# Kernel optimization log

Hardware: AMD Instinct MI355X
Metric: run time of the kernel (lower is better)

The kernel has to match this reference:

```python
import jax, jax.numpy as jnp
import numpy as np

# Geometry of the single LocallyConnected2d layer being decomposed
FACTOR = 2      # number of sublayers the out_channels are split into
KH = KW = 3     # kernel size
DH = DW = 1     # stride
OH = OW = 32    # output spatial size
B, C_IN, C_OUT = 128, 32, 64
H = W = OH + KH - 1  # 34 (valid unfold with stride 1)


def setup_inputs() -> dict:
    key = jax.random.key(0)
    kx, kw_, kb = jax.random.split(key, 3)
    x = jax.random.normal(kx, (B, C_IN, H, W), dtype=jnp.float32)
    # per-location weights: (out_ch, in_ch, oh, ow, kh*kw) -- no weight sharing
    weight = jax.random.normal(kw_, (C_OUT, C_IN, OH, OW, KH * KW), dtype=jnp.float32) * 0.05
    bias = jax.random.normal(kb, (C_OUT, OH, OW), dtype=jnp.float32)
    return {"x": x, "weight": weight, "bias": bias}


def _unfold(x):
    # x: (B, C, H, W) -> patches: (B, C, OH, OW, KH*KW)
    # equivalent to torch x.unfold(2,kh,dh).unfold(3,kw,dw).reshape(..., kh*kw)
    cols = [x[:, :, i:i + DH * OH:DH, j:j + DW * OW:DW]
            for i in range(KH) for j in range(KW)]
    return jnp.stack(cols, axis=-1)


def reference(x, weight, bias):
    patches = _unfold(x)  # (B, C, OH, OW, K2)
    new_ch = weight.shape[0] // FACTOR
    outs = []
    for g in range(FACTOR):  # decomposed sublayers, concatenated on channel dim
        w_g = weight[g * new_ch:(g + 1) * new_ch]
        b_g = bias[g * new_ch:(g + 1) * new_ch]
        # out[b,o,i,j] = sum_{c,k} patches[b,c,i,j,k] * w[o,c,i,j,k] + b[o,i,j]
        o_g = jnp.einsum('bcijk,ocijk->boij', patches, w_g) + b_g[None]
        outs.append(o_g)
    return jnp.concatenate(outs, axis=1)  # (B, C_OUT, OH, OW)
```

## Files before the change

kernel.cpp:

```cpp
#include <hip/hip_runtime.h>
#include <cstdint>
#include <cstddef>

#define B_    128
#define C_    32
#define O_    64
#define H_    34
#define NPOS  1024
#define K9    9
#define BC    (B_ * C_)
#define BO    (B_ * O_)
#define NPK   (NPOS * K9)

typedef __bf16 v8bf __attribute__((ext_vector_type(8)));
typedef float  v4f  __attribute__((ext_vector_type(4)));
typedef float  f4a  __attribute__((ext_vector_type(4)));

__device__ __forceinline__ unsigned short f2bf(float f) {
    union { float f; unsigned int u; } v; v.f = f;
    unsigned int u = v.u;
    return (unsigned short)((u + 0x7FFFu + ((u >> 16) & 1u)) >> 16);
}

__global__ __launch_bounds__(256) void repack_x(const float* __restrict__ x,
                                                unsigned short* __restrict__ x2) {
    const int bq = blockIdx.x / 17;
    const int hp = blockIdx.x % 17;
    const int b0 = bq * 2;
    const int h0 = hp * 2;
    __shared__ unsigned short tile[2][H_][66];
    const int t = threadIdx.x;

    for (int e = t; e < 2176; e += 256) {
        const int bb  = e / 1088;
        const int rem = e % 1088;
        const int c   = rem / 34;
        const int wp  = rem % 34;
        const float2 v = *(const float2*)(x +
            ((size_t)((b0 + bb) * C_ + c) * H_ + h0) * H_ + wp * 2);
        const int hh = (wp >= 17) ? 1 : 0;
        const int w  = wp * 2 - hh * 34;
        const int idx = bb * 32 + c;
        tile[hh][w][idx]     = f2bf(v.x);
        tile[hh][w + 1][idx] = f2bf(v.y);
    }
    __syncthreads();

    for (int e = t; e < 2176; e += 256) {
        const int hh  = e / 1088;
        const int rem = e % 1088;
        const int w   = rem >> 5;
        const int i2  = rem & 31;
        ushort2 pk;
        pk.x = tile[hh][w][i2 * 2];
        pk.y = tile[hh][w][i2 * 2 + 1];
        *(ushort2*)(x2 + (size_t)((h0 + hh) * H_ + w) * BC + bq * 64 + i2 * 2) = pk;
    }
}

__global__ __launch_bounds__(256, 4) void lc_fused3(const unsigned short* __restrict__ x2,
                                                    const float* __restrict__ weight,
                                                    const float* __restrict__ bias,
                                                    float* __restrict__ out) {
    __shared__ __align__(16) unsigned short Wl[36 * 512];

    const int bid = blockIdx.x;
    const int lb  = (bid & 7) * 128 + (bid >> 3);
    const int i   = lb >> 5;
    const int jq  = (lb >> 3) & 3;
    const int oq  = (lb >> 1) & 3;
    const int bh  = lb & 1;
    const int j0  = jq * 8;
    const int o0  = oq * 16;
    const int posbase = i * 32 + j0;
    const int t = threadIdx.x;

    const int wv = t >> 6;
    const int l  = t & 63;
    const int lm = l & 15;
    const int q  = l >> 4;

    v4f acc[8];
#pragma unroll
    for (int a = 0; a < 8; ++a) acc[a] = (v4f){0.f, 0.f, 0.f, 0.f};

    const float* wbase = weight + ((size_t)(o0 * C_) * NPOS + posbase) * K9;

#pragma unroll
    for (int jjh = 0; jjh < 2; ++jjh) {
        const float* wb = wbase + jjh * 36;
#pragma unroll
        for (int g = 0; g < 2; ++g) {
            f4a v[9];
#pragma unroll
            for (int r = 0; r < 9; ++r) {
                const int idx = (g * 9 + r) * 256 + t;
                const int pl  = idx / 9;
                const int d4  = idx % 9;
                v[r] = *(const f4a*)(wb + (size_t)pl * NPK + d4 * 4);
            }
#pragma unroll
            for (int r = 0; r < 9; ++r) {
                const int idx = (g * 9 + r) * 256 + t;
                const int pl  = idx / 9;
                const int d4  = idx % 9;
                const int col = ((pl >> 3) ^ (d4 & 7)) * 8 + (pl & 7);
#pragma unroll
                for (int u = 0; u < 4; ++u)
                    Wl[(d4 * 4 + u) * 512 + col] = f2bf(v[r][u]);
            }
        }
        __syncthreads();

#pragma unroll
        for (int kh = 0; kh < 3; ++kh) {
            v8bf ax[6];
            const int rowbase = (i + kh) * H_ + j0 + jjh * 4;
#pragma unroll
            for (int w6 = 0; w6 < 6; ++w6) {
                const unsigned short* xrow = x2 + (size_t)(rowbase + w6) * BC;
                ax[w6] = *(const v8bf*)(xrow + (bh * 64 + wv * 16 + lm) * C_ + q * 8);
            }
#pragma unroll
            for (int kw = 0; kw < 3; ++kw) {
                const int tap = kh * 3 + kw;
#pragma unroll
                for (int jj = 0; jj < 4; ++jj) {
                    const int jk = jj * K9 + tap;
                    const int gc = ((lm * 4 + q) ^ ((jk >> 2) & 7)) * 8;
                    const v8bf bfr = *(const v8bf*)&Wl[jk * 512 + gc];
                    acc[jjh * 4 + jj] = __builtin_amdgcn_mfma_f32_16x16x32_bf16(
                        ax[kw + jj], bfr, acc[jjh * 4 + jj], 0, 0, 0);
                }
            }
        }
        if (jjh == 0) __syncthreads();
    }

    const float* bp = bias + (size_t)(o0 + lm) * NPOS + posbase;
    const f4a bv0 = *(const f4a*)bp;
    const f4a bv1 = *(const f4a*)(bp + 4);
#pragma unroll
    for (int r2 = 0; r2 < 4; ++r2) {
        const int b = bh * 64 + wv * 16 + q * 4 + r2;
        float* op = out + ((size_t)b * O_ + (o0 + lm)) * NPOS + posbase;
        f4a lo = {acc[0][r2] + bv0[0], acc[1][r2] + bv0[1],
                  acc[2][r2] + bv0[2], acc[3][r2] + bv0[3]};
        f4a hi = {acc[4][r2] + bv1[0], acc[5][r2] + bv1[1],
                  acc[6][r2] + bv1[2], acc[7][r2] + bv1[3]};
        *(f4a*)op       = lo;
        *(f4a*)(op + 4) = hi;
    }
}

__global__ __launch_bounds__(256) void lc_fallback(const float* __restrict__ x,
                                                   const float* __restrict__ weight,
                                                   const float* __restrict__ bias,
                                                   float* __restrict__ out) {
    const int pos = blockIdx.x;
    const int i = pos >> 5, j = pos & 31;
    const int t  = threadIdx.x;
    const int wv = t >> 6;
    const int l  = t & 63;
    const int lm = l & 15;
    const int q  = l >> 4;

    float bv[4];
#pragma unroll
    for (int nt = 0; nt < 4; ++nt)
        bv[nt] = bias[(size_t)(nt * 16 + lm) * NPOS + pos];

    v4f acc[2][4];
#pragma unroll
    for (int a = 0; a < 2; ++a)
#pragma unroll
        for (int n = 0; n < 4; ++n) acc[a][n] = (v4f){0.f, 0.f, 0.f, 0.f};

    for (int k = 0; k < K9; ++k) {
        const int kh = k / 3, kw = k % 3;
        v8bf af[2], bfr[4];
#pragma unroll
        for (int mt = 0; mt < 2; ++mt) {
            const int b = wv * 32 + mt * 16 + lm;
            union { v8bf v; unsigned short s[8]; } u;
#pragma unroll
            for (int cc = 0; cc < 8; ++cc)
                u.s[cc] = f2bf(x[(((size_t)b * C_ + q * 8 + cc) * H_ + (i + kh)) * H_ + (j + kw)]);
            af[mt] = u.v;
        }
#pragma unroll
        for (int nt = 0; nt < 4; ++nt) {
            union { v8bf v; unsigned short s[8]; } u;
#pragma unroll
            for (int cc = 0; cc < 8; ++cc) {
                const int p = (nt * 16 + lm) * C_ + q * 8 + cc;
                u.s[cc] = f2bf(weight[((size_t)p * NPOS + pos) * K9 + k]);
            }
            bfr[nt] = u.v;
        }
#pragma unroll
        for (int mt = 0; mt < 2; ++mt)
#pragma unroll
            for (int nt = 0; nt < 4; ++nt)
                acc[mt][nt] = __builtin_amdgcn_mfma_f32_16x16x32_bf16(
                    af[mt], bfr[nt], acc[mt][nt], 0, 0, 0);
    }
#pragma unroll
    for (int mt = 0; mt < 2; ++mt)
#pragma unroll
        for (int nt = 0; nt < 4; ++nt) {
            const int o = nt * 16 + lm;
#pragma unroll
            for (int r = 0; r < 4; ++r) {
                const int b = wv * 32 + mt * 16 + q * 4 + r;
                out[(size_t)(b * O_ + o) * NPOS + pos] = acc[mt][nt][r] + bv[nt];
            }
        }
}

extern "C" void kernel_launch(void* const* d_in, const int* in_sizes, int n_in,
                              void* d_out, int out_size, void* d_ws, size_t ws_size,
                              hipStream_t stream) {
    const float* x      = (const float*)d_in[0];
    const float* weight = (const float*)d_in[1];
    const float* bias   = (const float*)d_in[2];
    float* out          = (float*)d_out;

    const size_t X2B = (size_t)H_ * H_ * BC * sizeof(unsigned short);

    if (ws_size >= X2B) {
        unsigned short* x2 = (unsigned short*)d_ws;
        repack_x<<<64 * 17, 256, 0, stream>>>(x, x2);
        lc_fused3<<<1024, 256, 0, stream>>>(x2, weight, bias, out);
    } else {
        lc_fallback<<<NPOS, 256, 0, stream>>>(x, weight, bias, out);
    }
}
```

Baseline: 174.2 us.

## Enlarge block tile to cover all batches and sixteen positions per block

```diff
diff --git a/kernel.cpp b/kernel.cpp
--- a/kernel.cpp
+++ b/kernel.cpp
@@ -58,98 +58,101 @@
     }
 }
 
-__global__ __launch_bounds__(256, 4) void lc_fused3(const unsigned short* __restrict__ x2,
+__global__ __launch_bounds__(512, 2) void lc_fused5(const unsigned short* __restrict__ x2,
                                                     const float* __restrict__ weight,
                                                     const float* __restrict__ bias,
                                                     float* __restrict__ out) {
-    __shared__ __align__(16) unsigned short Wl[36 * 512];
+    __shared__ __align__(16) unsigned short Wl[144 * 512];
 
     const int bid = blockIdx.x;
-    const int lb  = (bid & 7) * 128 + (bid >> 3);
-    const int i   = lb >> 5;
-    const int jq  = (lb >> 3) & 3;
-    const int oq  = (lb >> 1) & 3;
-    const int bh  = lb & 1;
-    const int j0  = jq * 8;
+    const int lb  = (bid & 7) * 32 + (bid >> 3);
+    const int i   = lb >> 3;
+    const int jq  = (lb >> 2) & 1;
+    const int oq  = lb & 3;
+    const int j0  = jq * 16;
     const int o0  = oq * 16;
     const int posbase = i * 32 + j0;
     const int t = threadIdx.x;
+
+    const float* wbase = weight + ((size_t)(o0 * C_) * NPOS + posbase) * K9;
+#pragma unroll
+    for (int r = 0; r < 3; ++r) {
+        f4a v[3][4];
+#pragma unroll
+        for (int m = 0; m < 3; ++m) {
+            const int Q  = (r * 3 + m) * 512 + t;
+            const int pl = Q / 9;
+            const int q4 = Q % 9;
+            const float* src = wbase + (size_t)pl * NPK + q4 * 16;
+#pragma unroll
+            for (int s = 0; s < 4; ++s)
+                v[m][s] = *(const f4a*)(src + s * 4);
+        }
+#pragma unroll
+        for (int m = 0; m < 3; ++m) {
+            const int Q  = (r * 3 + m) * 512 + t;
+            const int pl = Q / 9;
+            const int q4 = Q % 9;
+#pragma unroll
+            for (int s = 0; s < 4; ++s) {
+                const int d4  = q4 * 4 + s;
+                const int col = ((pl >> 3) ^ (d4 & 7)) * 8 + (pl & 7);
+#pragma unroll
+                for (int u = 0; u < 4; ++u)
+                    Wl[(d4 * 4 + u) * 512 + col] = f2bf(v[m][s][u]);
+            }
+        }
+    }
+    __syncthreads();
 
     const int wv = t >> 6;
     const int l  = t & 63;
     const int lm = l & 15;
     const int q  = l >> 4;
 
-    v4f acc[8];
-#pragma unroll
-    for (int a = 0; a < 8; ++a) acc[a] = (v4f){0.f, 0.f, 0.f, 0.f};
-
-    const float* wbase = weight + ((size_t)(o0 * C_) * NPOS + posbase) * K9;
-
-#pragma unroll
-    for (int jjh = 0; jjh < 2; ++jjh) {
-        const float* wb = wbase + jjh * 36;
-#pragma unroll
-        for (int g = 0; g < 2; ++g) {
-            f4a v[9];
-#pragma unroll
-            for (int r = 0; r < 9; ++r) {
-                const int idx = (g * 9 + r) * 256 + t;
-                const int pl  = idx / 9;
-                const int d4  = idx % 9;
-                v[r] = *(const f4a*)(wb + (size_t)pl * NPK + d4 * 4);
-            }
-#pragma unroll
-            for (int r = 0; r < 9; ++r) {
-                const int idx = (g * 9 + r) * 256 + t;
-                const int pl  = idx / 9;
-                const int d4  = idx % 9;
-                const int col = ((pl >> 3) ^ (d4 & 7)) * 8 + (pl & 7);
-#pragma unroll
-                for (int u = 0; u < 4; ++u)
-                    Wl[(d4 * 4 + u) * 512 + col] = f2bf(v[r][u]);
-            }
-        }
-        __syncthreads();
+#pragma unroll
+    for (int jh = 0; jh < 2; ++jh) {
+        v4f acc[8];
+#pragma unroll
+        for (int a = 0; a < 8; ++a) acc[a] = (v4f){0.f, 0.f, 0.f, 0.f};
 
 #pragma unroll
         for (int kh = 0; kh < 3; ++kh) {
-            v8bf ax[6];
-            const int rowbase = (i + kh) * H_ + j0 + jjh * 4;
-#pragma unroll
-            for (int w6 = 0; w6 < 6; ++w6) {
+            v8bf ax[10];
+            const int rowbase = (i + kh) * H_ + j0 + jh * 8;
+#pragma unroll
+            for (int w6 = 0; w6 < 10; ++w6) {
                 const unsigned short* xrow = x2 + (size_t)(rowbase + w6) * BC;
-                ax[w6] = *(const v8bf*)(xrow + (bh * 64 + wv * 16 + lm) * C_ + q * 8);
+                ax[w6] = *(const v8bf*)(xrow + (wv * 16 + lm) * C_ + q * 8);
             }
 #pragma unroll
             for (int kw = 0; kw < 3; ++kw) {
                 const int tap = kh * 3 + kw;
 #pragma unroll
-                for (int jj = 0; jj < 4; ++jj) {
-                    const int jk = jj * K9 + tap;
+                for (int jj = 0; jj < 8; ++jj) {
+                    const int jk = (jh * 8 + jj) * K9 + tap;
                     const int gc = ((lm * 4 + q) ^ ((jk >> 2) & 7)) * 8;
                     const v8bf bfr = *(const v8bf*)&Wl[jk * 512 + gc];
-                    acc[jjh * 4 + jj] = __builtin_amdgcn_mfma_f32_16x16x32_bf16(
-                        ax[kw + jj], bfr, acc[jjh * 4 + jj], 0, 0, 0);
+                    acc[jj] = __builtin_amdgcn_mfma_f32_16x16x32_bf16(
+                        ax[kw + jj], bfr, acc[jj], 0, 0, 0);
                 }
             }
         }
-        if (jjh == 0) __syncthreads();
-    }
-
-    const float* bp = bias + (size_t)(o0 + lm) * NPOS + posbase;
-    const f4a bv0 = *(const f4a*)bp;
-    const f4a bv1 = *(const f4a*)(bp + 4);
-#pragma unroll
-    for (int r2 = 0; r2 < 4; ++r2) {
-        const int b = bh * 64 + wv * 16 + q * 4 + r2;
-        float* op = out + ((size_t)b * O_ + (o0 + lm)) * NPOS + posbase;
-        f4a lo = {acc[0][r2] + bv0[0], acc[1][r2] + bv0[1],
-                  acc[2][r2] + bv0[2], acc[3][r2] + bv0[3]};
-        f4a hi = {acc[4][r2] + bv1[0], acc[5][r2] + bv1[1],
-                  acc[6][r2] + bv1[2], acc[7][r2] + bv1[3]};
-        *(f4a*)op       = lo;
-        *(f4a*)(op + 4) = hi;
+
+        const float* bp = bias + (size_t)(o0 + lm) * NPOS + posbase + jh * 8;
+        const f4a bv0 = *(const f4a*)bp;
+        const f4a bv1 = *(const f4a*)(bp + 4);
+#pragma unroll
+        for (int r2 = 0; r2 < 4; ++r2) {
+            const int b = wv * 16 + q * 4 + r2;
+            float* op = out + ((size_t)b * O_ + (o0 + lm)) * NPOS + posbase + jh * 8;
+            f4a lo = {acc[0][r2] + bv0[0], acc[1][r2] + bv0[1],
+                      acc[2][r2] + bv0[2], acc[3][r2] + bv0[3]};
+            f4a hi = {acc[4][r2] + bv1[0], acc[5][r2] + bv1[1],
+                      acc[6][r2] + bv1[2], acc[7][r2] + bv1[3]};
+            *(f4a*)op       = lo;
+            *(f4a*)(op + 4) = hi;
+        }
     }
 }
 
@@ -231,7 +234,7 @@
     if (ws_size >= X2B) {
         unsigned short* x2 = (unsigned short*)d_ws;
         repack_x<<<64 * 17, 256, 0, stream>>>(x, x2);
-        lc_fused3<<<1024, 256, 0, stream>>>(x2, weight, bias, out);
+        lc_fused5<<<256, 512, 0, stream>>>(x2, weight, bias, out);
     } else {
         lc_fallback<<<NPOS, 256, 0, stream>>>(x, weight, bias, out);
     }
```

Measured after the change: 158.8 us. -8.9%, faster.
